# Performance work log

Hardware: AMD Instinct MI355X
Metric: run time of the kernel (lower is better)

Reference implementation:

```python
import jax, jax.numpy as jnp
import numpy as np
import math

B, S, H, NH = 4, 4096, 1024, 1
HD = H // NH
D_FF = 4 * H
R = 2  # number of causal rules
SPARSITY = 0.9
LN_EPS = 1e-5


def setup_inputs() -> dict:
    key = jax.random.key(0)
    ks = jax.random.split(key, 16)
    n = lambda k, shp, s=0.02: jax.random.normal(k, shp, dtype=jnp.float32) * s
    return {
        "x": jax.random.normal(ks[0], (B, S, H), dtype=jnp.float32),
        "attention_mask": jnp.ones((B, S), dtype=bool),
        # attention projections (torch Linear convention: weight [out, in])
        "wq": n(ks[1], (H, H)), "bq": jnp.zeros((H,), jnp.float32),
        "wk": n(ks[2], (H, H)), "bk": jnp.zeros((H,), jnp.float32),
        "wv": n(ks[3], (H, H)), "bv": jnp.zeros((H,), jnp.float32),
        "wo": n(ks[4], (H, H)), "bo": jnp.zeros((H,), jnp.float32),
        # layer norms
        "ln1_g": jnp.ones((H,), jnp.float32), "ln1_b": jnp.zeros((H,), jnp.float32),
        "ln2_g": jnp.ones((H,), jnp.float32), "ln2_b": jnp.zeros((H,), jnp.float32),
        # sparse FFN
        "fc1_w": n(ks[5], (D_FF, H)), "fc1_b": jnp.zeros((D_FF,), jnp.float32),
        "fc2_w": n(ks[6], (H, D_FF)), "fc2_b": jnp.zeros((H,), jnp.float32),
        "router_w": n(ks[7], (D_FF, H)), "router_b": jnp.zeros((D_FF,), jnp.float32),
        # causal biasing network: per rule, cause extractor Linear(H,1) and effect predictor Linear(1,H)
        "cause_w": n(ks[8], (R, H)), "cause_b": jnp.zeros((R,), jnp.float32),
        "eff_w": n(ks[9], (R, H)), "eff_b": jnp.zeros((R, H), jnp.float32),
        "strengths": jnp.array([0.8, 0.5], dtype=jnp.float32),
    }


def _ln(x, g, b):
    m = jnp.mean(x, axis=-1, keepdims=True)
    v = jnp.mean((x - m) ** 2, axis=-1, keepdims=True)
    return (x - m) / jnp.sqrt(v + LN_EPS) * g + b


def reference(x, attention_mask, wq, bq, wk, bk, wv, bv, wo, bo,
              ln1_g, ln1_b, ln2_g, ln2_b, fc1_w, fc1_b, fc2_w, fc2_b,
              router_w, router_b, cause_w, cause_b, eff_w, eff_b, strengths):
    # --- attention sub-block ---
    h1 = _ln(x, ln1_g, ln1_b)
    q = (jnp.einsum('bsh,oh->bso', h1, wq) + bq).reshape(B, S, NH, HD).transpose(0, 2, 1, 3)
    k = (jnp.einsum('bsh,oh->bso', h1, wk) + bk).reshape(B, S, NH, HD).transpose(0, 2, 1, 3)
    v = (jnp.einsum('bsh,oh->bso', h1, wv) + bv).reshape(B, S, NH, HD).transpose(0, 2, 1, 3)
    scores = jnp.einsum('bhqd,bhkd->bhqk', q, k) / math.sqrt(HD)  # [B,NH,S,S]
    causal = jnp.triu(jnp.ones((S, S), dtype=bool), 1)
    scores = jnp.where(causal[None, None], jnp.float32(-10000.0), scores)
    scores = jnp.where(~attention_mask[:, None, None, :], jnp.float32(-10000.0), scores)
    # rule-based causal bias: sum_r (effect_emb_r @ h1^T)
    cs = jnp.einsum('bsh,rh->rbs', h1, cause_w) + cause_b[:, None, None]      # [R,B,S]
    exp_eff = cs * strengths[:, None, None]                                   # [R,B,S]
    eff = exp_eff[..., None] * eff_w[:, None, None, :] + eff_b[:, None, None, :]  # [R,B,S,H]
    bias = jnp.einsum('rbsh,bth->bst', eff, h1)                               # [B,S,S], sums rules
    bias = bias.reshape(B, S, NH, S).transpose(0, 2, 1, 3)                    # valid since NH==1
    scores = scores + bias
    attn = jax.nn.softmax(scores, axis=-1)
    ctx = jnp.einsum('bhqk,bhkd->bhqd', attn, v).transpose(0, 2, 1, 3).reshape(B, S, H)
    x = x + jnp.einsum('bsh,oh->bso', ctx, wo) + bo
    # --- sparse FFN sub-block ---
    h2 = _ln(x, ln2_g, ln2_b)
    ff = jax.nn.gelu(jnp.einsum('bsh,fh->bsf', h2, fc1_w) + fc1_b, approximate=False)
    logits = jnp.einsum('bsh,fh->bsf', h2, router_w) + router_b
    k_top = max(1, int(D_FF * (1.0 - SPARSITY)))  # 409
    _, idx = jax.lax.top_k(logits.reshape(B * S, D_FF), k_top)
    rows = jnp.arange(B * S)[:, None]
    mask = jnp.zeros((B * S, D_FF), jnp.float32).at[rows, idx].set(1.0).reshape(B, S, D_FF)
    x = x + jnp.einsum('bsf,hf->bsh', ff * mask, fc2_w) + fc2_b
    return (x, attn)
```

## Files before the change

### kernel.cpp

```cpp
#include <hip/hip_runtime.h>


typedef unsigned short ushortT;
typedef short bf16x8 __attribute__((ext_vector_type(8)));
typedef float f32x4 __attribute__((ext_vector_type(4)));
typedef unsigned short us8 __attribute__((ext_vector_type(8)));

#define SEQ 4096
#define HDIM 1024
#define TOK 16384
#define DFF 4096
#define KTOP 409

__device__ __forceinline__ float b2f(unsigned short u) {
    return __uint_as_float(((unsigned)u) << 16);
}
__device__ __forceinline__ unsigned short f2b(float f) {
    unsigned u = __float_as_uint(f);
    u += 0x7fffu + ((u >> 16) & 1u);
    return (unsigned short)(u >> 16);
}

__device__ __forceinline__ float blkRedF(float v, float* red4) {
    #pragma unroll
    for (int o = 32; o; o >>= 1) v += __shfl_xor(v, o);
    if ((threadIdx.x & 63) == 0) red4[threadIdx.x >> 6] = v;
    __syncthreads();
    v = red4[0] + red4[1] + red4[2] + red4[3];
    __syncthreads();
    return v;
}
__device__ __forceinline__ int blkRedI(int v, int* red4) {
    #pragma unroll
    for (int o = 32; o; o >>= 1) v += __shfl_xor(v, o);
    if ((threadIdx.x & 63) == 0) red4[threadIdx.x >> 6] = v;
    __syncthreads();
    v = red4[0] + red4[1] + red4[2] + red4[3];
    __syncthreads();
    return v;
}

template<int HASLO>
__global__ __launch_bounds__(256) void cvt2_k(const float* __restrict__ s,
                                              ushortT* __restrict__ hi,
                                              ushortT* __restrict__ lo) {
    const int i = (blockIdx.x * 256 + threadIdx.x) * 4;
    float4 v = *(const float4*)(s + i);
    float vv[4] = {v.x, v.y, v.z, v.w};
    ushort4 h, l;
    unsigned short* hp = &h.x; unsigned short* lp = &l.x;
    #pragma unroll
    for (int j = 0; j < 4; ++j) {
        hp[j] = f2b(vv[j]);
        if constexpr (HASLO) lp[j] = f2b(vv[j] - b2f(hp[j]));
    }
    *(ushort4*)(hi + i) = h;
    if constexpr (HASLO) *(ushort4*)(lo + i) = l;
}

__global__ __launch_bounds__(256) void ln_k(const float* __restrict__ in,
                                            ushortT* __restrict__ ohi,
                                            ushortT* __restrict__ olo,
                                            const float* __restrict__ g,
                                            const float* __restrict__ b) {
    __shared__ float red4[4];
    const long long row = blockIdx.x;
    const int t = threadIdx.x;
    float4 v = ((const float4*)(in + row * HDIM))[t];
    float x[4] = {v.x, v.y, v.z, v.w};
    float s = x[0] + x[1] + x[2] + x[3];
    s = blkRedF(s, red4);
    const float mean = s * (1.0f / HDIM);
    float vs = 0.f;
    #pragma unroll
    for (int k2 = 0; k2 < 4; ++k2) { float d = x[k2] - mean; vs += d * d; }
    vs = blkRedF(vs, red4);
    const float inv = 1.0f / sqrtf(vs * (1.0f / HDIM) + 1e-5f);
    float4 gv = ((const float4*)g)[t];
    float4 bv = ((const float4*)b)[t];
    float o[4];
    o[0] = (x[0] - mean) * inv * gv.x + bv.x;
    o[1] = (x[1] - mean) * inv * gv.y + bv.y;
    o[2] = (x[2] - mean) * inv * gv.z + bv.z;
    o[3] = (x[3] - mean) * inv * gv.w + bv.w;
    ushort4 h, l;
    unsigned short* hp = &h.x; unsigned short* lp = &l.x;
    #pragma unroll
    for (int j = 0; j < 4; ++j) {
        hp[j] = f2b(o[j]);
        lp[j] = f2b(o[j] - b2f(hp[j]));
    }
    ((ushort4*)(ohi + row * HDIM))[t] = h;
    ((ushort4*)(olo + row * HDIM))[t] = l;
}

__global__ __launch_bounds__(256) void bias_pre(const ushortT* __restrict__ hhi,
        const ushortT* __restrict__ hlo,
        const float* __restrict__ cw, const float* __restrict__ cb,
        const float* __restrict__ ew, const float* __restrict__ eb,
        const float* __restrict__ st,
        float* __restrict__ e0, float* __restrict__ e1,
        float* __restrict__ uu, float* __restrict__ ww, float* __restrict__ zz) {
    const int tok = blockIdx.x * 4 + (threadIdx.x >> 6);
    const int L = threadIdx.x & 63;
    const long long base = (long long)tok * HDIM + L * 16;
    us8 h0 = *(const us8*)(hhi + base);
    us8 h1v = *(const us8*)(hhi + base + 8);
    us8 l0 = *(const us8*)(hlo + base);
    us8 l1v = *(const us8*)(hlo + base + 8);
    float hv[16];
    #pragma unroll
    for (int q = 0; q < 8; ++q) {
        hv[q] = b2f(h0[q]) + b2f(l0[q]);
        hv[8 + q] = b2f(h1v[q]) + b2f(l1v[q]);
    }
    float d0 = 0, d1 = 0, du = 0, dw = 0, dz = 0;
    #pragma unroll
    for (int q = 0; q < 16; ++q) {
        d0 += hv[q] * cw[L * 16 + q];
        d1 += hv[q] * cw[HDIM + L * 16 + q];
        du += hv[q] * ew[L * 16 + q];
        dw += hv[q] * ew[HDIM + L * 16 + q];
        dz += hv[q] * (eb[L * 16 + q] + eb[HDIM + L * 16 + q]);
    }
    #pragma unroll
    for (int o = 32; o; o >>= 1) {
        d0 += __shfl_xor(d0, o); d1 += __shfl_xor(d1, o);
        du += __shfl_xor(du, o); dw += __shfl_xor(dw, o); dz += __shfl_xor(dz, o);
    }
    if (L == 0) {
        e0[tok] = (d0 + cb[0]) * st[0];
        e1[tok] = (d1 + cb[1]) * st[1];
        uu[tok] = du; ww[tok] = dw; zz[tok] = dz;
    }
}

__global__ __launch_bounds__(256) void row_sum(const float* __restrict__ e,
                                               float* __restrict__ l) {
    __shared__ float red4[4];
    const int r = blockIdx.x;
    const int s = r & 4095;
    const float* rowp = e + (long long)r * SEQ;
    const int c0 = threadIdx.x * 16;
    float sum = 0.f;
    if (c0 + 15 <= s) {
        const float4* p = (const float4*)(rowp + c0);
        #pragma unroll
        for (int i = 0; i < 4; ++i) {
            float4 v = p[i];
            sum += v.x + v.y + v.z + v.w;
        }
    } else if (c0 <= s) {
        #pragma unroll
        for (int i = 0; i < 4; ++i) {
            float q0 = (c0 + i * 4 + 0 <= s) ? rowp[c0 + i * 4 + 0] : 0.f;
            float q1 = (c0 + i * 4 + 1 <= s) ? rowp[c0 + i * 4 + 1] : 0.f;
            float q2 = (c0 + i * 4 + 2 <= s) ? rowp[c0 + i * 4 + 2] : 0.f;
            float q3 = (c0 + i * 4 + 3 <= s) ? rowp[c0 + i * 4 + 3] : 0.f;
            sum += q0 + q1 + q2 + q3;
        }
    }
    sum = blkRedF(sum, red4);
    if (threadIdx.x == 0) l[r] = sum;
}

__global__ __launch_bounds__(256) void attn_norm(float* __restrict__ attn,
                                                 const float* __restrict__ l) {
    const long long g = (long long)blockIdx.x * 256 + threadIdx.x;
    const long long base = g * 8;
    const int r = (int)(base >> 12);
    const int s = r & 4095;
    const int c = (int)(base & 4095);
    float4 z = {0.f, 0.f, 0.f, 0.f};
    if (c > s) {
        *(float4*)(attn + base) = z;
        *(float4*)(attn + base + 4) = z;
        return;
    }
    const float inv = 1.0f / l[r];
    float4 v0 = *(const float4*)(attn + base);
    float4 v1 = *(const float4*)(attn + base + 4);
    if (c + 7 <= s) {
        v0.x *= inv; v0.y *= inv; v0.z *= inv; v0.w *= inv;
        v1.x *= inv; v1.y *= inv; v1.z *= inv; v1.w *= inv;
    } else {
        float vv[8] = {v0.x, v0.y, v0.z, v0.w, v1.x, v1.y, v1.z, v1.w};
        #pragma unroll
        for (int j = 0; j < 8; ++j) vv[j] = (c + j <= s) ? vv[j] * inv : 0.f;
        v0.x = vv[0]; v0.y = vv[1]; v0.z = vv[2]; v0.w = vv[3];
        v1.x = vv[4]; v1.y = vv[5]; v1.z = vv[6]; v1.w = vv[7];
    }
    *(float4*)(attn + base) = v0;
    *(float4*)(attn + base + 4) = v1;
}

__global__ __launch_bounds__(256) void topk_mask(const float* __restrict__ logits,
                                                 ushortT* __restrict__ ff) {
    __shared__ int red4[4];
    __shared__ int sc[256];
    const long long row = blockIdx.x;
    const int t = threadIdx.x;
    const float* lg = logits + row * (long long)DFF + t * 16;
    unsigned key[16];
    #pragma unroll
    for (int q4 = 0; q4 < 4; ++q4) {
        float4 v = ((const float4*)lg)[q4];
        float vv[4] = {v.x, v.y, v.z, v.w};
        #pragma unroll
        for (int j = 0; j < 4; ++j) {
            unsigned u = __float_as_uint(vv[j]);
            key[q4 * 4 + j] = (u & 0x80000000u) ? ~u : (u | 0x80000000u);
        }
    }
    unsigned T = 0;
    for (int bit = 31; bit >= 0; --bit) {
        unsigned cand = T | (1u << bit);
        int c = 0;
        #pragma unroll
        for (int q = 0; q < 16; ++q) c += (key[q] >= cand);
        c = blkRedI(c, red4);
        if (c >= KTOP) T = cand;
    }
    int cg = 0, eq = 0;
    #pragma unroll
    for (int q = 0; q < 16; ++q) { cg += (key[q] > T); eq += (key[q] == T); }
    cg = blkRedI(cg, red4);
    const int need = KTOP - cg;
    sc[t] = eq;
    __syncthreads();
    for (int o = 1; o < 256; o <<= 1) {
        int x = (t >= o) ? sc[t - o] : 0;
        __syncthreads();
        sc[t] += x;
        __syncthreads();
    }
    int pre = sc[t] - eq;
    ushortT* fr = ff + row * (long long)DFF + t * 16;
    #pragma unroll
    for (int q = 0; q < 16; ++q) {
        bool sel = (key[q] > T) || ((key[q] == T) && (pre < need));
        if (key[q] == T) pre++;
        if (!sel) fr[q] = 0;
    }
}

struct GemmP {
    const ushortT* A; const ushortT* A2; const float* Af;
    const ushortT* B; const ushortT* B2;
    long long aBatch, bBatch, oBatch;
    int lda, ldb, K, ldo;
    void* out; void* out2;
    const float* biasN; const float* biasN2; const float* biasM;
    const float *pe0, *pe1, *pu, *pw, *pz, *pl;
    const float* resF32;
    float scale;
    int nSplit;
};

template<int EPI, int AMODE, int BMODE>
__global__ __launch_bounds__(256) void gemm_nt(GemmP p) {
    __shared__ ushortT Ahi[4096];
    __shared__ ushortT Bhi[4096];
    __shared__ ushortT Alo[(AMODE >= 2) ? 4096 : 8];
    __shared__ ushortT Blo[(BMODE == 1) ? 4096 : 8];
    const int tid = threadIdx.x;
    const int L = tid & 63;
    const int w = tid >> 6;
    const int wm = w >> 1, wn = w & 1;
    int bn = blockIdx.x, bm = blockIdx.y;
    const int bz = blockIdx.z;
    {
        const int nx = gridDim.x;
        const int n = nx * gridDim.y;
        if ((n & 7) == 0) {
            const int id = bm * nx + bn;
            const int nid = (id & 7) * (n >> 3) + (id >> 3);
            bn = nid % nx; bm = nid / nx;
        }
    }

    f32x4 acc[4][4] = {};

    const long long obase = (long long)bz * p.oBatch;
    float* Of = (float*)p.out;
    ushortT* Oh = (ushortT*)p.out;
    ushortT* Ol = (ushortT*)p.out2;

    int gnv[4];
    #pragma unroll
    for (int j = 0; j < 4; ++j) gnv[j] = bn * 128 + wn * 64 + j * 16 + (L & 15);

    if constexpr (EPI == 2) {
        if (bn > bm) return;
    }

    int kEnd = p.K;
    if constexpr (EPI == 3) { kEnd = min(p.K, (bm + 1) * 128); }

    const int r0row = tid >> 2;
    const int r1row = 64 + r0row;
    const int rc   = ((tid & 3) ^ ((tid >> 3) & 3)) * 8;
    const int qsw  = (((L >> 4) ^ ((L >> 1) & 3))) * 8;

    for (int k0 = 0; k0 < kEnd; k0 += 32) {
        if constexpr (AMODE != 2) {
            const ushortT* Ab = p.A + (long long)bz * p.aBatch
                              + (long long)bm * 128 * p.lda + k0 + rc;
            __builtin_amdgcn_global_load_lds(
                (const __attribute__((address_space(1))) void*)(Ab + (long long)r0row * p.lda),
                (__attribute__((address_space(3))) void*)(Ahi + w * 512), 16, 0, 0);
            __builtin_amdgcn_global_load_lds(
                (const __attribute__((address_space(1))) void*)(Ab + (long long)r1row * p.lda),
                (__attribute__((address_space(3))) void*)(Ahi + 2048 + w * 512), 16, 0, 0);
            if constexpr (AMODE == 3) {
                const ushortT* Ab2 = p.A2 + (long long)bz * p.aBatch
                                   + (long long)bm * 128 * p.lda + k0 + rc;
                __builtin_amdgcn_global_load_lds(
                    (const __attribute__((address_space(1))) void*)(Ab2 + (long long)r0row * p.lda),
                    (__attribute__((address_space(3))) void*)(Alo + w * 512), 16, 0, 0);
                __builtin_amdgcn_global_load_lds(
                    (const __attribute__((address_space(1))) void*)(Ab2 + (long long)r1row * p.lda),
                    (__attribute__((address_space(3))) void*)(Alo + 2048 + w * 512), 16, 0, 0);
            }
        } else {
            const int arow = tid >> 1;
            const float* ap = p.Af + (long long)bz * p.aBatch
                            + ((long long)bm * 128 + arow) * p.lda
                            + k0 + (tid & 1) * 16;
            #pragma unroll
            for (int cc = 0; cc < 2; ++cc) {
                const int c = (tid & 1) * 2 + cc;
                const int cs = (c ^ ((arow >> 1) & 3)) * 8;
                float4 v0 = ((const float4*)ap)[cc * 2];
                float4 v1 = ((const float4*)ap)[cc * 2 + 1];
                float vv[8] = {v0.x, v0.y, v0.z, v0.w, v1.x, v1.y, v1.z, v1.w};
                us8 h, l;
                #pragma unroll
                for (int j = 0; j < 8; ++j) {
                    h[j] = f2b(vv[j]);
                    l[j] = f2b(vv[j] - b2f(h[j]));
                }
                *(us8*)(Ahi + arow * 32 + cs) = h;
                *(us8*)(Alo + arow * 32 + cs) = l;
            }
        }
        {
            const ushortT* Bb = p.B + (long long)bz * p.bBatch
                              + (long long)bn * 128 * p.ldb + k0 + rc;
            __builtin_amdgcn_global_load_lds(
                (const __attribute__((address_space(1))) void*)(Bb + (long long)r0row * p.ldb),
                (__attribute__((address_space(3))) void*)(Bhi + w * 512), 16, 0, 0);
            __builtin_amdgcn_global_load_lds(
                (const __attribute__((address_space(1))) void*)(Bb + (long long)r1row * p.ldb),
                (__attribute__((address_space(3))) void*)(Bhi + 2048 + w * 512), 16, 0, 0);
            if constexpr (BMODE == 1) {
                const ushortT* Bb2 = p.B2 + (long long)bz * p.bBatch
                                   + (long long)bn * 128 * p.ldb + k0 + rc;
                __builtin_amdgcn_global_load_lds(
                    (const __attribute__((address_space(1))) void*)(Bb2 + (long long)r0row * p.ldb),
                    (__attribute__((address_space(3))) void*)(Blo + w * 512), 16, 0, 0);
                __builtin_amdgcn_global_load_lds(
                    (const __attribute__((address_space(1))) void*)(Bb2 + (long long)r1row * p.ldb),
                    (__attribute__((address_space(3))) void*)(Blo + 2048 + w * 512), 16, 0, 0);
            }
        }
        __syncthreads();
        {
            bf16x8 ah[4], bh[4];
            #pragma unroll
            for (int i = 0; i < 4; ++i)
                ah[i] = *(const bf16x8*)(Ahi + (wm * 64 + i * 16 + (L & 15)) * 32 + qsw);
            #pragma unroll
            for (int j = 0; j < 4; ++j)
                bh[j] = *(const bf16x8*)(Bhi + (wn * 64 + j * 16 + (L & 15)) * 32 + qsw);
            #pragma unroll
            for (int i = 0; i < 4; ++i)
                #pragma unroll
                for (int j = 0; j < 4; ++j)
                    acc[i][j] = __builtin_amdgcn_mfma_f32_16x16x32_bf16(ah[i], bh[j], acc[i][j], 0, 0, 0);
            if constexpr (BMODE == 1) {
                bf16x8 bl[4];
                #pragma unroll
                for (int j = 0; j < 4; ++j)
                    bl[j] = *(const bf16x8*)(Blo + (wn * 64 + j * 16 + (L & 15)) * 32 + qsw);
                #pragma unroll
                for (int i = 0; i < 4; ++i)
                    #pragma unroll
                    for (int j = 0; j < 4; ++j)
                        acc[i][j] = __builtin_amdgcn_mfma_f32_16x16x32_bf16(ah[i], bl[j], acc[i][j], 0, 0, 0);
            }
            if constexpr (AMODE >= 2) {
                bf16x8 al[4];
                #pragma unroll
                for (int i = 0; i < 4; ++i)
                    al[i] = *(const bf16x8*)(Alo + (wm * 64 + i * 16 + (L & 15)) * 32 + qsw);
                #pragma unroll
                for (int i = 0; i < 4; ++i)
                    #pragma unroll
                    for (int j = 0; j < 4; ++j)
                        acc[i][j] = __builtin_amdgcn_mfma_f32_16x16x32_bf16(al[i], bh[j], acc[i][j], 0, 0, 0);
            }
        }
        __syncthreads();
    }

    float c0[4], c1[4], c2[4];
    #pragma unroll
    for (int j = 0; j < 4; ++j) {
        if constexpr (EPI == 2) {
            c0[j] = p.pu[bz * SEQ + gnv[j]];
            c1[j] = p.pw[bz * SEQ + gnv[j]];
            c2[j] = p.pz[bz * SEQ + gnv[j]];
        } else if constexpr (EPI == 6) {
            c0[j] = (gnv[j] < p.nSplit) ? p.biasN[gnv[j]]
                                        : p.biasN2[gnv[j] - p.nSplit];
        } else if constexpr (EPI == 4 || EPI == 5 || EPI == 9) {
            c0[j] = p.biasN[gnv[j]];
        }
    }

    #pragma unroll
    for (int i = 0; i < 4; ++i) {
        #pragma unroll
        for (int r = 0; r < 4; ++r) {
            const int gm = bm * 128 + wm * 64 + i * 16 + ((L >> 4) << 2) + r;
            float rA = 0.f, rB = 0.f, mult = 1.f;
            if constexpr (EPI == 2) { rA = p.pe0[bz * SEQ + gm]; rB = p.pe1[bz * SEQ + gm]; }
            if constexpr (EPI == 3) mult = 1.0f / p.pl[bz * SEQ + gm];
            if constexpr (EPI == 8) rA = p.biasM[gm];
            #pragma unroll
            for (int j = 0; j < 4; ++j) {
                float v = acc[i][j][r];
                const long long oidx = obase + (long long)gm * p.ldo + gnv[j];
                if constexpr (EPI == 2) {
                    float s = v * p.scale + rA * c0[j] + rB * c1[j] + c2[j];
                    Of[oidx] = (gnv[j] <= gm) ? __expf(s) : 0.f;
                } else if constexpr (EPI == 3) {
                    float val = v * mult;
                    ushortT h = f2b(val);
                    Oh[oidx] = h; Ol[oidx] = f2b(val - b2f(h));
                } else if constexpr (EPI == 4) {
                    Of[oidx] = v + c0[j] + p.resF32[(long long)gm * p.ldo + gnv[j]];
                } else if constexpr (EPI == 5) {
                    float tt = v + c0[j];
                    Oh[oidx] = f2b(0.5f * tt * (1.0f + erff(tt * 0.70710678118654752f)));
                } else if constexpr (EPI == 6) {
                    float val = v + c0[j];
                    ushortT h = f2b(val);
                    Oh[oidx] = h; Ol[oidx] = f2b(val - b2f(h));
                } else if constexpr (EPI == 8) {
                    float val = v + rA;
                    ushortT h = f2b(val);
                    Oh[oidx] = h; Ol[oidx] = f2b(val - b2f(h));
                } else if constexpr (EPI == 9) {
                    Of[oidx] = v + c0[j];
                }
            }
        }
    }
}

extern "C" void kernel_launch(void* const* d_in, const int* in_sizes, int n_in,
                              void* d_out, int out_size, void* d_ws, size_t ws_size,
                              hipStream_t stream) {
    (void)in_sizes; (void)n_in; (void)out_size; (void)ws_size;
    const float* x    = (const float*)d_in[0];
    const float* wq   = (const float*)d_in[2];
    const float* bq   = (const float*)d_in[3];
    const float* wk   = (const float*)d_in[4];
    const float* bk   = (const float*)d_in[5];
    const float* wv   = (const float*)d_in[6];
    const float* bv   = (const float*)d_in[7];
    const float* wo   = (const float*)d_in[8];
    const float* bo   = (const float*)d_in[9];
    const float* ln1g = (const float*)d_in[10];
    const float* ln1b = (const float*)d_in[11];
    const float* ln2g = (const float*)d_in[12];
    const float* ln2b = (const float*)d_in[13];
    const float* fc1w = (const float*)d_in[14];
    const float* fc1b = (const float*)d_in[15];
    const float* fc2w = (const float*)d_in[16];
    const float* fc2b = (const float*)d_in[17];
    const float* rww  = (const float*)d_in[18];
    const float* rwb  = (const float*)d_in[19];
    const float* cw   = (const float*)d_in[20];
    const float* cb   = (const float*)d_in[21];
    const float* ew   = (const float*)d_in[22];
    const float* eb   = (const float*)d_in[23];
    const float* st   = (const float*)d_in[24];

    char* ws = (char*)d_ws;
    const size_t MB32 = 33554432;
    ushortT* h1hi = (ushortT*)(ws + 0 * MB32);
    ushortT* h1lo = (ushortT*)(ws + 1 * MB32);
    ushortT* qkhi = (ushortT*)(ws + 2 * MB32);
    ushortT* qklo = (ushortT*)(ws + 4 * MB32);
    ushortT* vthi = (ushortT*)(ws + 6 * MB32);
    ushortT* vtlo = (ushortT*)(ws + 7 * MB32);
    ushortT* wqkh = (ushortT*)(ws + 6 * MB32);
    ushortT* wqkl = wqkh + 2 * (size_t)(HDIM * HDIM);
    ushortT* ctxhi = (ushortT*)(ws + 2 * MB32);
    ushortT* ctxlo = (ushortT*)(ws + 3 * MB32);
    float*   x1   = (float*)(ws + 0 * MB32);
    ushortT* h2hi = (ushortT*)(ws + 4 * MB32);
    ushortT* h2lo = (ushortT*)(ws + 5 * MB32);
    ushortT* fw   = vthi;
    float*   logc = (float*)(ws + 2 * MB32);
    ushortT* ffc  = (ushortT*)(ws + 7 * MB32);
    char* tail = ws + 8 * MB32;
    ushortT* whi = (ushortT*)(tail);
    ushortT* wlo = (ushortT*)(tail + 2097152);
    char* sm = tail + 4194304;
    float* e0v = (float*)(sm);
    float* e1v = (float*)(sm + 1 * 65536);
    float* uu  = (float*)(sm + 2 * 65536);
    float* wwp = (float*)(sm + 3 * 65536);
    float* zz  = (float*)(sm + 4 * 65536);
    float* lrow = (float*)(sm + 5 * 65536);

    const int NW = HDIM * HDIM;
    const int NF = DFF * HDIM;
    ushortT* fc1h = fw;
    ushortT* fc2h = fw + 1 * (size_t)NF;
    ushortT* rwh  = fw + 2 * (size_t)NF;
    ushortT* rwl  = fw + 3 * (size_t)NF;

    float* outx = (float*)d_out;
    float* attn = outx + (size_t)TOK * HDIM;

    ln_k<<<TOK, 256, 0, stream>>>(x, h1hi, h1lo, ln1g, ln1b);

    cvt2_k<1><<<NW / 1024, 256, 0, stream>>>(wq, wqkh, wqkl);
    cvt2_k<1><<<NW / 1024, 256, 0, stream>>>(wk, wqkh + NW, wqkl + NW);
    GemmP pq{};
    pq.A = h1hi; pq.A2 = h1lo; pq.B = wqkh; pq.B2 = wqkl;
    pq.lda = HDIM; pq.ldb = HDIM; pq.K = HDIM; pq.ldo = 2048;
    pq.out = qkhi; pq.out2 = qklo;
    pq.biasN = bq; pq.biasN2 = bk; pq.nSplit = 1024;
    gemm_nt<6, 3, 1><<<dim3(16, 128, 1), 256, 0, stream>>>(pq);

    cvt2_k<1><<<NW / 1024, 256, 0, stream>>>(wv, whi, wlo);
    GemmP pv{};
    pv.A = whi; pv.A2 = wlo; pv.B = h1hi; pv.B2 = h1lo;
    pv.lda = HDIM; pv.ldb = HDIM; pv.K = HDIM; pv.ldo = SEQ;
    pv.aBatch = 0; pv.bBatch = (long long)SEQ * HDIM; pv.oBatch = (long long)HDIM * SEQ;
    pv.out = vthi; pv.out2 = vtlo; pv.biasM = bv;
    gemm_nt<8, 3, 1><<<dim3(32, 8, 4), 256, 0, stream>>>(pv);

    bias_pre<<<4096, 256, 0, stream>>>(h1hi, h1lo, cw, cb, ew, eb, st, e0v, e1v, uu, wwp, zz);

    GemmP ps{};
    ps.A = qkhi; ps.A2 = qklo; ps.B = qkhi + 1024; ps.B2 = qklo + 1024;
    ps.lda = 2048; ps.ldb = 2048; ps.K = HDIM; ps.ldo = SEQ;
    ps.aBatch = (long long)SEQ * 2048; ps.bBatch = (long long)SEQ * 2048;
    ps.oBatch = (long long)SEQ * SEQ;
    ps.out = attn; ps.scale = 0.03125f;
    ps.pe0 = e0v; ps.pe1 = e1v; ps.pu = uu; ps.pw = wwp; ps.pz = zz;
    gemm_nt<2, 3, 1><<<dim3(32, 32, 4), 256, 0, stream>>>(ps);

    row_sum<<<TOK, 256, 0, stream>>>(attn, lrow);

    GemmP pp{};
    pp.Af = attn; pp.B = vthi; pp.B2 = vtlo;
    pp.lda = SEQ; pp.ldb = SEQ; pp.K = SEQ; pp.ldo = HDIM;
    pp.aBatch = (long long)SEQ * SEQ; pp.bBatch = (long long)HDIM * SEQ;
    pp.oBatch = (long long)SEQ * HDIM;
    pp.out = ctxhi; pp.out2 = ctxlo; pp.pl = lrow;
    gemm_nt<3, 2, 1><<<dim3(8, 32, 4), 256, 0, stream>>>(pp);

    attn_norm<<<32768, 256, 0, stream>>>(attn, lrow);

    cvt2_k<1><<<NW / 1024, 256, 0, stream>>>(wo, whi, wlo);
    GemmP po{};
    po.A = ctxhi; po.A2 = ctxlo; po.B = whi; po.B2 = wlo;
    po.lda = HDIM; po.ldb = HDIM; po.K = HDIM; po.ldo = HDIM;
    po.out = x1; po.biasN = bo; po.resF32 = x;
    gemm_nt<4, 3, 1><<<dim3(8, 128, 1), 256, 0, stream>>>(po);

    ln_k<<<TOK, 256, 0, stream>>>(x1, h2hi, h2lo, ln2g, ln2b);

    cvt2_k<0><<<NF / 1024, 256, 0, stream>>>(fc1w, fc1h, nullptr);
    cvt2_k<0><<<NF / 1024, 256, 0, stream>>>(fc2w, fc2h, nullptr);
    cvt2_k<1><<<NF / 1024, 256, 0, stream>>>(rww, rwh, rwl);

    for (int c = 0; c < 4; ++c) {
        const size_t roff = (size_t)c * 4096 * HDIM;
        GemmP pf{};
        pf.A = h2hi + roff; pf.B = fc1h;
        pf.lda = HDIM; pf.ldb = HDIM; pf.K = HDIM; pf.ldo = DFF;
        pf.out = ffc; pf.biasN = fc1b;
        gemm_nt<5, 0, 0><<<dim3(32, 32, 1), 256, 0, stream>>>(pf);

        GemmP pr{};
        pr.A = h2hi + roff; pr.A2 = h2lo + roff; pr.B = rwh; pr.B2 = rwl;
        pr.lda = HDIM; pr.ldb = HDIM; pr.K = HDIM; pr.ldo = DFF;
        pr.out = logc; pr.biasN = rwb;
        gemm_nt<9, 3, 1><<<dim3(32, 32, 1), 256, 0, stream>>>(pr);

        topk_mask<<<4096, 256, 0, stream>>>(logc, ffc);

        GemmP p2{};
        p2.A = ffc; p2.B = fc2h; p2.lda = DFF; p2.ldb = DFF; p2.K = DFF; p2.ldo = HDIM;
        p2.out = outx + roff; p2.biasN = fc2b;
        p2.resF32 = x1 + roff;
        gemm_nt<4, 0, 0><<<dim3(8, 32, 1), 256, 0, stream>>>(p2);
    }
}
```

Baseline: 3.106 ms.

## Double-buffer GEMM LDS tiles and drop block-swizzle remap

Converts the GEMM main loop to a two-stage LDS double buffer: the next k-tile is issued into the alternate buffer before the current tile's MFMAs, with one barrier per iteration instead of two. The goal is to overlap global-to-LDS loads with matrix math. It also removes the grouped block-index remapping, which may lower L2 reuse, and replaces the round-to-nearest hi-part split with truncation for fp32 A operands. The doubled LDS footprint can lower occupancy.

```diff
diff --git a/kernel.cpp b/kernel.cpp
--- a/kernel.cpp
+++ b/kernel.cpp
@@ -259,25 +259,15 @@
 
 template<int EPI, int AMODE, int BMODE>
 __global__ __launch_bounds__(256) void gemm_nt(GemmP p) {
-    __shared__ ushortT Ahi[4096];
-    __shared__ ushortT Bhi[4096];
-    __shared__ ushortT Alo[(AMODE >= 2) ? 4096 : 8];
-    __shared__ ushortT Blo[(BMODE == 1) ? 4096 : 8];
+    __shared__ ushortT Ahi[2][4096];
+    __shared__ ushortT Bhi[2][4096];
+    __shared__ ushortT Alo[(AMODE >= 2) ? 2 : 1][(AMODE >= 2) ? 4096 : 8];
+    __shared__ ushortT Blo[(BMODE == 1) ? 2 : 1][(BMODE == 1) ? 4096 : 8];
     const int tid = threadIdx.x;
     const int L = tid & 63;
     const int w = tid >> 6;
     const int wm = w >> 1, wn = w & 1;
-    int bn = blockIdx.x, bm = blockIdx.y;
-    const int bz = blockIdx.z;
-    {
-        const int nx = gridDim.x;
-        const int n = nx * gridDim.y;
-        if ((n & 7) == 0) {
-            const int id = bm * nx + bn;
-            const int nid = (id & 7) * (n >> 3) + (id >> 3);
-            bn = nid % nx; bm = nid / nx;
-        }
-    }
+    const int bn = blockIdx.x, bm = blockIdx.y, bz = blockIdx.z;
 
     f32x4 acc[4][4] = {};
 
@@ -296,31 +286,32 @@
 
     int kEnd = p.K;
     if constexpr (EPI == 3) { kEnd = min(p.K, (bm + 1) * 128); }
+    const int nt = kEnd >> 5;
 
     const int r0row = tid >> 2;
     const int r1row = 64 + r0row;
     const int rc   = ((tid & 3) ^ ((tid >> 3) & 3)) * 8;
     const int qsw  = (((L >> 4) ^ ((L >> 1) & 3))) * 8;
 
-    for (int k0 = 0; k0 < kEnd; k0 += 32) {
+    auto STAGE = [&](int sb, int k0) {
         if constexpr (AMODE != 2) {
             const ushortT* Ab = p.A + (long long)bz * p.aBatch
                               + (long long)bm * 128 * p.lda + k0 + rc;
             __builtin_amdgcn_global_load_lds(
                 (const __attribute__((address_space(1))) void*)(Ab + (long long)r0row * p.lda),
-                (__attribute__((address_space(3))) void*)(Ahi + w * 512), 16, 0, 0);
+                (__attribute__((address_space(3))) void*)(&Ahi[sb][w * 512]), 16, 0, 0);
             __builtin_amdgcn_global_load_lds(
                 (const __attribute__((address_space(1))) void*)(Ab + (long long)r1row * p.lda),
-                (__attribute__((address_space(3))) void*)(Ahi + 2048 + w * 512), 16, 0, 0);
+                (__attribute__((address_space(3))) void*)(&Ahi[sb][2048 + w * 512]), 16, 0, 0);
             if constexpr (AMODE == 3) {
                 const ushortT* Ab2 = p.A2 + (long long)bz * p.aBatch
                                    + (long long)bm * 128 * p.lda + k0 + rc;
                 __builtin_amdgcn_global_load_lds(
                     (const __attribute__((address_space(1))) void*)(Ab2 + (long long)r0row * p.lda),
-                    (__attribute__((address_space(3))) void*)(Alo + w * 512), 16, 0, 0);
+                    (__attribute__((address_space(3))) void*)(&Alo[sb][w * 512]), 16, 0, 0);
                 __builtin_amdgcn_global_load_lds(
                     (const __attribute__((address_space(1))) void*)(Ab2 + (long long)r1row * p.lda),
-                    (__attribute__((address_space(3))) void*)(Alo + 2048 + w * 512), 16, 0, 0);
+                    (__attribute__((address_space(3))) void*)(&Alo[sb][2048 + w * 512]), 16, 0, 0);
             }
         } else {
             const int arow = tid >> 1;
@@ -337,11 +328,11 @@
                 us8 h, l;
                 #pragma unroll
                 for (int j = 0; j < 8; ++j) {
-                    h[j] = f2b(vv[j]);
+                    h[j] = (ushortT)(__float_as_uint(vv[j]) >> 16);
                     l[j] = f2b(vv[j] - b2f(h[j]));
                 }
-                *(us8*)(Ahi + arow * 32 + cs) = h;
-                *(us8*)(Alo + arow * 32 + cs) = l;
+                *(us8*)(&Ahi[sb][arow * 32 + cs]) = h;
+                *(us8*)(&Alo[sb][arow * 32 + cs]) = l;
             }
         }
         {
@@ -349,30 +340,36 @@
                               + (long long)bn * 128 * p.ldb + k0 + rc;
             __builtin_amdgcn_global_load_lds(
                 (const __attribute__((address_space(1))) void*)(Bb + (long long)r0row * p.ldb),
-                (__attribute__((address_space(3))) void*)(Bhi + w * 512), 16, 0, 0);
+                (__attribute__((address_space(3))) void*)(&Bhi[sb][w * 512]), 16, 0, 0);
             __builtin_amdgcn_global_load_lds(
                 (const __attribute__((address_space(1))) void*)(Bb + (long long)r1row * p.ldb),
-                (__attribute__((address_space(3))) void*)(Bhi + 2048 + w * 512), 16, 0, 0);
+                (__attribute__((address_space(3))) void*)(&Bhi[sb][2048 + w * 512]), 16, 0, 0);
             if constexpr (BMODE == 1) {
                 const ushortT* Bb2 = p.B2 + (long long)bz * p.bBatch
                                    + (long long)bn * 128 * p.ldb + k0 + rc;
                 __builtin_amdgcn_global_load_lds(
                     (const __attribute__((address_space(1))) void*)(Bb2 + (long long)r0row * p.ldb),
-                    (__attribute__((address_space(3))) void*)(Blo + w * 512), 16, 0, 0);
+                    (__attribute__((address_space(3))) void*)(&Blo[sb][w * 512]), 16, 0, 0);
                 __builtin_amdgcn_global_load_lds(
                     (const __attribute__((address_space(1))) void*)(Bb2 + (long long)r1row * p.ldb),
-                    (__attribute__((address_space(3))) void*)(Blo + 2048 + w * 512), 16, 0, 0);
+                    (__attribute__((address_space(3))) void*)(&Blo[sb][2048 + w * 512]), 16, 0, 0);
             }
         }
-        __syncthreads();
+    };
+
+    STAGE(0, 0);
+    __syncthreads();
+    int cur = 0;
+    for (int t = 0; ; ) {
+        if (t + 1 < nt) STAGE(cur ^ 1, (t + 1) << 5);
         {
             bf16x8 ah[4], bh[4];
             #pragma unroll
             for (int i = 0; i < 4; ++i)
-                ah[i] = *(const bf16x8*)(Ahi + (wm * 64 + i * 16 + (L & 15)) * 32 + qsw);
+                ah[i] = *(const bf16x8*)(&Ahi[cur][(wm * 64 + i * 16 + (L & 15)) * 32 + qsw]);
             #pragma unroll
             for (int j = 0; j < 4; ++j)
-                bh[j] = *(const bf16x8*)(Bhi + (wn * 64 + j * 16 + (L & 15)) * 32 + qsw);
+                bh[j] = *(const bf16x8*)(&Bhi[cur][(wn * 64 + j * 16 + (L & 15)) * 32 + qsw]);
             #pragma unroll
             for (int i = 0; i < 4; ++i)
                 #pragma unroll
@@ -382,7 +379,7 @@
                 bf16x8 bl[4];
                 #pragma unroll
                 for (int j = 0; j < 4; ++j)
-                    bl[j] = *(const bf16x8*)(Blo + (wn * 64 + j * 16 + (L & 15)) * 32 + qsw);
+                    bl[j] = *(const bf16x8*)(&Blo[cur][(wn * 64 + j * 16 + (L & 15)) * 32 + qsw]);
                 #pragma unroll
                 for (int i = 0; i < 4; ++i)
                     #pragma unroll
@@ -393,7 +390,7 @@
                 bf16x8 al[4];
                 #pragma unroll
                 for (int i = 0; i < 4; ++i)
-                    al[i] = *(const bf16x8*)(Alo + (wm * 64 + i * 16 + (L & 15)) * 32 + qsw);
+                    al[i] = *(const bf16x8*)(&Alo[cur][(wm * 64 + i * 16 + (L & 15)) * 32 + qsw]);
                 #pragma unroll
                 for (int i = 0; i < 4; ++i)
                     #pragma unroll
@@ -401,7 +398,10 @@
                         acc[i][j] = __builtin_amdgcn_mfma_f32_16x16x32_bf16(al[i], bh[j], acc[i][j], 0, 0, 0);
             }
         }
+        ++t;
+        if (t >= nt) break;
         __syncthreads();
+        cur ^= 1;
     }
 
     float c0[4], c1[4], c2[4];
```

New measurement: 3.234 ms. 4.1% more time.
